# Performance work log

Hardware: AMD Instinct MI355X
Metric: run time of the kernel (lower is better)

The kernel has to match this reference:

```python
import jax, jax.numpy as jnp
import numpy as np

DIM = 768
NUM_HEADS = 1
AGENT_NUM = 4
HEAD_DIM = DIM // NUM_HEADS
SCALE = HEAD_DIM ** -0.5
B, N = 128, 196


def setup_inputs() -> dict:
    key = jax.random.key(0)
    ks = jax.random.split(key, 12)
    s = 0.02
    return {
        "x": jax.random.normal(ks[0], (B, N, DIM), jnp.float32),
        "attn_1": jax.random.normal(ks[1], (B, NUM_HEADS, AGENT_NUM, N), jnp.float32),
        "attn_2": jax.random.normal(ks[2], (B, NUM_HEADS, AGENT_NUM, N), jnp.float32),
        "agent_tk1": jax.random.normal(ks[3], (B, NUM_HEADS, AGENT_NUM, HEAD_DIM), jnp.float32),
        "agent_tk2": jax.random.normal(ks[4], (B, NUM_HEADS, AGENT_NUM, HEAD_DIM), jnp.float32),
        "W_qkv": jax.random.normal(ks[5], (DIM, 3 * DIM), jnp.float32) * s,
        "W_pool1": jax.random.normal(ks[6], (DIM, DIM // 2), jnp.float32) * s,
        "b_pool1": jnp.zeros((DIM // 2,), jnp.float32),
        "W_pool2": jax.random.normal(ks[7], (DIM // 2, NUM_HEADS * AGENT_NUM * DIM), jnp.float32) * s,
        "b_pool2": jnp.zeros((NUM_HEADS * AGENT_NUM * DIM,), jnp.float32),
        "W_proj": jax.random.normal(ks[8], (DIM, DIM), jnp.float32) * s,
        "b_proj": jnp.zeros((DIM,), jnp.float32),
    }


def reference(x, attn_1, attn_2, agent_tk1, agent_tk2,
              W_qkv, W_pool1, b_pool1, W_pool2, b_pool2, W_proj, b_proj):
    b, n, c = x.shape
    # qkv projection: (b, n, 3c) -> q, k, v each (b, n, c)
    qkv = x @ W_qkv
    q, k, v = jnp.split(qkv, 3, axis=-1)

    # agent tokens via pooling MLP on q (exact-erf GELU like torch nn.GELU)
    pooled = jax.nn.gelu(q @ W_pool1 + b_pool1, approximate=False) @ W_pool2 + b_pool2
    # mean over tokens -> (b, num_heads*agent_num*dim) == (b, agent_num*dim) since num_heads==1
    agent_tokens = pooled.mean(axis=1).reshape(b, AGENT_NUM, NUM_HEADS, HEAD_DIM)
    agent_tokens = agent_tokens.transpose(0, 2, 1, 3)  # (b, h, a, d)

    # split heads: (b, h, n, d)
    q = q.reshape(b, n, NUM_HEADS, HEAD_DIM).transpose(0, 2, 1, 3)
    k = k.reshape(b, n, NUM_HEADS, HEAD_DIM).transpose(0, 2, 1, 3)
    v = v.reshape(b, n, NUM_HEADS, HEAD_DIM).transpose(0, 2, 1, 3)

    # stage 1: agent attends to keys -> (b, h, a, n)
    agent_attn = jax.nn.softmax(jnp.einsum("bhad,bhnd->bhan", agent_tokens * SCALE, k), axis=-1)
    agent_rep = agent_attn

    # softmax blending with externally provided attn maps
    s = attn_1 + attn_2
    agent_attn = (agent_attn * jax.nn.softmax(s, axis=-1)
                  + agent_attn * jax.nn.softmax(s, axis=1)
                  + agent_attn) / 3.0

    agent_v = jnp.einsum("bhan,bhnd->bhad", agent_attn, v)  # (b, h, a, d)

    # blend agent tokens with external agent tokens
    t = agent_tk1 + agent_tk2
    agent_tokens = (agent_tokens * jax.nn.softmax(t, axis=-1)
                    + agent_tokens * jax.nn.softmax(t, axis=1)
                    + agent_tokens) / 3.0

    # stage 2: queries attend to agents -> (b, h, n, a)
    q_attn = jax.nn.softmax(jnp.einsum("bhnd,bhad->bhna", q * SCALE, agent_tokens), axis=-1)
    out = jnp.einsum("bhna,bhad->bhnd", q_attn, agent_v)  # (b, h, n, d)

    out = out.transpose(0, 2, 1, 3).reshape(b, n, c)
    out = out @ W_proj + b_proj
    return (out, agent_rep, agent_tokens)
```

## Files before the change

kernel.cpp:

```cpp
#include <hip/hip_runtime.h>
#include <hip/hip_bf16.h>
#include <math.h>

#define NB    128
#define NTOK  196
#define DIMC  768
#define AGN   4
#define SCALE_F 0.036084391824351614f

typedef __bf16  bf16x8  __attribute__((ext_vector_type(8)));
typedef float   f32x4   __attribute__((ext_vector_type(4)));
typedef unsigned short ushortx8 __attribute__((ext_vector_type(8)));
typedef unsigned short ushortx4 __attribute__((ext_vector_type(4)));

__device__ __forceinline__ unsigned short f2bf(float f) {
    union { float f; unsigned int u; } v; v.f = f;
    unsigned int r = v.u + 0x7fffu + ((v.u >> 16) & 1u);
    return (unsigned short)(r >> 16);
}
__device__ __forceinline__ float bf2f(unsigned short u) {
    union { unsigned int u; float f; } v; v.u = ((unsigned int)u) << 16;
    return v.f;
}
__device__ __forceinline__ void load_lds16(const void* g, void* l) {
    __builtin_amdgcn_global_load_lds(
        (const __attribute__((address_space(1))) unsigned int*)g,
        (__attribute__((address_space(3))) unsigned int*)l, 16, 0, 0);
}

template<int EPI>
__global__ __launch_bounds__(256) void gemm_bf16_k(
    const unsigned short* __restrict__ A, int lda,
    const unsigned short* __restrict__ Bt, int ldb,
    const float* __restrict__ bias,
    float* __restrict__ Cf, unsigned short* __restrict__ Cbf,
    int ldc, int K)
{
    __shared__ alignas(16) char lds[16384];

    const int tid  = threadIdx.x;
    const int lane = tid & 63;
    const int wv   = tid >> 6;
    const int wr   = wv >> 1, wc = wv & 1;
    const int row0 = blockIdx.y * 128;
    const int col0 = blockIdx.x * 128;

    const int c0 = wv * 2, c1 = wv * 2 + 1;
    const int srow = lane >> 2;
    const int skel = (lane & 3) << 3;
    const unsigned short* Ag0 = A  + (size_t)(row0 + c0*16 + srow) * lda + skel;
    const unsigned short* Ag1 = A  + (size_t)(row0 + c1*16 + srow) * lda + skel;
    const unsigned short* Bg0 = Bt + (size_t)(col0 + c0*16 + srow) * ldb + skel;
    const unsigned short* Bg1 = Bt + (size_t)(col0 + c1*16 + srow) * ldb + skel;
    char* lA0 = lds + c0 * 1024;
    char* lA1 = lds + c1 * 1024;
    char* lB0 = lds + 8192 + c0 * 1024;
    char* lB1 = lds + 8192 + c1 * 1024;

    f32x4 acc[4][4];
    #pragma unroll
    for (int m = 0; m < 4; m++)
        #pragma unroll
        for (int n = 0; n < 4; n++) acc[m][n] = (f32x4){0.f, 0.f, 0.f, 0.f};

    const int frow = lane & 15;
    const int kgrp = (lane >> 4) * 16;

    for (int bk = 0; bk < K; bk += 32) {
        __syncthreads();
        load_lds16(Ag0 + bk, lA0);
        load_lds16(Ag1 + bk, lA1);
        load_lds16(Bg0 + bk, lB0);
        load_lds16(Bg1 + bk, lB1);
        __syncthreads();

        bf16x8 af[4], bf[4];
        #pragma unroll
        for (int m = 0; m < 4; m++)
            af[m] = *(const bf16x8*)(lds + ((wr*64 + m*16 + frow) * 64 + kgrp));
        #pragma unroll
        for (int n = 0; n < 4; n++)
            bf[n] = *(const bf16x8*)(lds + 8192 + ((wc*64 + n*16 + frow) * 64 + kgrp));
        #pragma unroll
        for (int m = 0; m < 4; m++)
            #pragma unroll
            for (int n = 0; n < 4; n++)
                acc[m][n] = __builtin_amdgcn_mfma_f32_16x16x32_bf16(af[m], bf[n], acc[m][n], 0, 0, 0);
    }

    const int crow = (lane >> 4) << 2;
    #pragma unroll
    for (int n = 0; n < 4; n++) {
        const int col = col0 + wc*64 + n*16 + frow;
        const float bn = (EPI > 0) ? bias[col] : 0.f;
        #pragma unroll
        for (int m = 0; m < 4; m++) {
            #pragma unroll
            for (int r = 0; r < 4; r++) {
                const int row = row0 + wr*64 + m*16 + crow + r;
                float v = acc[m][n][r];
                if (EPI > 0) v += bn;
                if (EPI == 2) v = 0.5f * v * (1.f + erff(v * 0.7071067811865476f));
                if (EPI == 0) Cbf[(size_t)row * ldc + col] = f2bf(v);
                else          Cf [(size_t)row * ldc + col] = v;
            }
        }
    }
}

__global__ __launch_bounds__(256) void conv_k(const float* __restrict__ in,
                                              unsigned short* __restrict__ out)
{
    const size_t i = ((size_t)blockIdx.x * 256 + threadIdx.x) * 8;
    float4 v0 = *(const float4*)(in + i);
    float4 v1 = *(const float4*)(in + i + 4);
    ushortx8 o;
    o[0]=f2bf(v0.x); o[1]=f2bf(v0.y); o[2]=f2bf(v0.z); o[3]=f2bf(v0.w);
    o[4]=f2bf(v1.x); o[5]=f2bf(v1.y); o[6]=f2bf(v1.z); o[7]=f2bf(v1.w);
    *(ushortx8*)(out + i) = o;
}

__global__ __launch_bounds__(256) void tconv_k(const float* __restrict__ W,
                                               unsigned short* __restrict__ Wt,
                                               int K, int N)
{
    __shared__ float t[32][33];
    const int n0 = blockIdx.x * 32, k0 = blockIdx.y * 32;
    const int r = threadIdx.x >> 3;
    const int c = (threadIdx.x & 7) * 4;
    float4 v = *(const float4*)&W[(size_t)(k0 + r) * N + n0 + c];
    t[r][c] = v.x; t[r][c+1] = v.y; t[r][c+2] = v.z; t[r][c+3] = v.w;
    __syncthreads();
    ushortx4 o;
    o[0] = f2bf(t[c+0][r]); o[1] = f2bf(t[c+1][r]);
    o[2] = f2bf(t[c+2][r]); o[3] = f2bf(t[c+3][r]);
    *(ushortx4*)&Wt[(size_t)(n0 + r) * K + k0 + c] = o;
}

__global__ __launch_bounds__(384) void mean_k(const float* __restrict__ h1,
                                              float* __restrict__ mh)
{
    const int b = blockIdx.x, j = threadIdx.x;
    const float* p = h1 + (size_t)b * NTOK * 384 + j;
    float s = 0.f;
    for (int n = 0; n < NTOK; n++) s += p[(size_t)n * 384];
    mh[b * 384 + j] = s * (1.f / (float)NTOK);
}

__global__ __launch_bounds__(256) void pool2_k(const float* __restrict__ mh,
                                               const float* __restrict__ W2,
                                               const float* __restrict__ b2,
                                               float* __restrict__ ab)
{
    __shared__ float rows[8][384];
    const int tid = threadIdx.x;
    const int bb0 = blockIdx.y * 8;
    for (int i = tid; i < 8 * 384; i += 256)
        rows[i / 384][i % 384] = mh[(size_t)(bb0 + i / 384) * 384 + (i % 384)];
    __syncthreads();

    const int j = blockIdx.x * 256 + tid;
    const float bj = b2[j];
    float acc[8];
    #pragma unroll
    for (int r = 0; r < 8; r++) acc[r] = bj;
    for (int k = 0; k < 384; k++) {
        float w = W2[(size_t)k * 3072 + j];
        #pragma unroll
        for (int r = 0; r < 8; r++) acc[r] = fmaf(rows[r][k], w, acc[r]);
    }
    #pragma unroll
    for (int r = 0; r < 8; r++) ab[(size_t)(bb0 + r) * 3072 + j] = acc[r];
}

__device__ __forceinline__ float wred_max(float v) {
    #pragma unroll
    for (int o = 32; o; o >>= 1) v = fmaxf(v, __shfl_xor(v, o, 64));
    return v;
}
__device__ __forceinline__ float wred_sum(float v) {
    #pragma unroll
    for (int o = 32; o; o >>= 1) v += __shfl_xor(v, o, 64);
    return v;
}

__global__ __launch_bounds__(256) void stage1_k(
    const unsigned short* __restrict__ qkv, const float* __restrict__ agent_base,
    const float* __restrict__ attn1, const float* __restrict__ attn2,
    const float* __restrict__ tk1, const float* __restrict__ tk2,
    float* __restrict__ agent_v, float* __restrict__ at_blend,
    float* __restrict__ out_rep, float* __restrict__ out_at)
{
    __shared__ float at_s[AGN * DIMC];
    __shared__ float sc[AGN][NTOK];
    __shared__ float s2[AGN][NTOK];

    const int b = blockIdx.x, tid = threadIdx.x;
    for (int i = tid; i < AGN * DIMC; i += 256) at_s[i] = agent_base[(size_t)b * 3072 + i];
    __syncthreads();

    if (tid < NTOK) {
        const unsigned short* krow = qkv + (size_t)(b * NTOK + tid) * 2304 + 768;
        float s[AGN] = {0.f, 0.f, 0.f, 0.f};
        for (int d = 0; d < DIMC; d += 8) {
            ushortx8 kv = *(const ushortx8*)(krow + d);
            float kf[8];
            #pragma unroll
            for (int e = 0; e < 8; e++) kf[e] = bf2f(kv[e]);
            #pragma unroll
            for (int a = 0; a < AGN; a++) {
                const float* ap = at_s + a * DIMC + d;
                float t = 0.f;
                #pragma unroll
                for (int e = 0; e < 8; e++) t = fmaf(ap[e], kf[e], t);
                s[a] += t;
            }
        }
        #pragma unroll
        for (int a = 0; a < AGN; a++) {
            sc[a][tid] = s[a] * SCALE_F;
            s2[a][tid] = attn1[(size_t)(b*AGN + a)*NTOK + tid] + attn2[(size_t)(b*AGN + a)*NTOK + tid];
        }
    }
    __syncthreads();

    const int w = tid >> 6, l = tid & 63;
    {
        const int a = w;
        float m = -1e30f;
        for (int i = l; i < NTOK; i += 64) m = fmaxf(m, sc[a][i]);
        m = wred_max(m);
        float ss = 0.f;
        for (int i = l; i < NTOK; i += 64) { float e = expf(sc[a][i] - m); sc[a][i] = e; ss += e; }
        ss = wred_sum(ss);
        float inv = 1.f / ss;
        for (int i = l; i < NTOK; i += 64) {
            float p = sc[a][i] * inv;
            sc[a][i] = p;
            out_rep[(size_t)(b*AGN + a)*NTOK + i] = p;
        }
        float m2 = -1e30f;
        for (int i = l; i < NTOK; i += 64) m2 = fmaxf(m2, s2[a][i]);
        m2 = wred_max(m2);
        float ss2 = 0.f;
        for (int i = l; i < NTOK; i += 64) { float e = expf(s2[a][i] - m2); s2[a][i] = e; ss2 += e; }
        ss2 = wred_sum(ss2);
        float inv2 = 1.f / ss2;
        for (int i = l; i < NTOK; i += 64)
            s2[a][i] = sc[a][i] * (s2[a][i] * inv2 + 2.f) * (1.f / 3.f);
    }
    __syncthreads();

    for (int d = tid; d < DIMC; d += 256) {
        float av[AGN] = {0.f, 0.f, 0.f, 0.f};
        const unsigned short* vcol = qkv + (size_t)b * NTOK * 2304 + 1536 + d;
        for (int n = 0; n < NTOK; n++) {
            float vv = bf2f(vcol[(size_t)n * 2304]);
            #pragma unroll
            for (int a = 0; a < AGN; a++) av[a] = fmaf(s2[a][n], vv, av[a]);
        }
        #pragma unroll
        for (int a = 0; a < AGN; a++) agent_v[(size_t)(b*AGN + a)*DIMC + d] = av[a];
    }

    {
        const int a = w;
        float tv[12];
        float m = -1e30f;
        #pragma unroll
        for (int i = 0; i < 12; i++) {
            int d = l + i * 64;
            tv[i] = tk1[(size_t)(b*AGN + a)*DIMC + d] + tk2[(size_t)(b*AGN + a)*DIMC + d];
            m = fmaxf(m, tv[i]);
        }
        m = wred_max(m);
        float ss = 0.f;
        #pragma unroll
        for (int i = 0; i < 12; i++) { tv[i] = expf(tv[i] - m); ss += tv[i]; }
        ss = wred_sum(ss);
        float inv = 1.f / ss;
        #pragma unroll
        for (int i = 0; i < 12; i++) {
            int d = l + i * 64;
            float ab = at_s[a*DIMC + d] * (tv[i] * inv + 2.f) * (1.f / 3.f);
            at_blend[(size_t)(b*AGN + a)*DIMC + d] = ab;
            out_at[(size_t)(b*AGN + a)*DIMC + d] = ab;
        }
    }
}

__global__ __launch_bounds__(256) void stage2_k(
    const unsigned short* __restrict__ qkv, const float* __restrict__ at_blend,
    const float* __restrict__ agent_v, unsigned short* __restrict__ out_attn_bf)
{
    __shared__ float atb[AGN * DIMC];
    __shared__ float av[AGN * DIMC];
    __shared__ float qa[NTOK][AGN];

    const int b = blockIdx.x, tid = threadIdx.x;
    for (int i = tid; i < AGN * DIMC; i += 256) {
        atb[i] = at_blend[(size_t)b * 3072 + i];
        av[i]  = agent_v[(size_t)b * 3072 + i];
    }
    __syncthreads();

    if (tid < NTOK) {
        const unsigned short* qrow = qkv + (size_t)(b * NTOK + tid) * 2304;
        float s[AGN] = {0.f, 0.f, 0.f, 0.f};
        for (int d = 0; d < DIMC; d += 8) {
            ushortx8 qv = *(const ushortx8*)(qrow + d);
            float qf[8];
            #pragma unroll
            for (int e = 0; e < 8; e++) qf[e] = bf2f(qv[e]);
            #pragma unroll
            for (int a = 0; a < AGN; a++) {
                const float* ap = atb + a * DIMC + d;
                float t = 0.f;
                #pragma unroll
                for (int e = 0; e < 8; e++) t = fmaf(ap[e], qf[e], t);
                s[a] += t;
            }
        }
        #pragma unroll
        for (int a = 0; a < AGN; a++) s[a] *= SCALE_F;
        float m = fmaxf(fmaxf(s[0], s[1]), fmaxf(s[2], s[3]));
        float e[AGN]; float ss = 0.f;
        #pragma unroll
        for (int a = 0; a < AGN; a++) { e[a] = expf(s[a] - m); ss += e[a]; }
        float inv = 1.f / ss;
        #pragma unroll
        for (int a = 0; a < AGN; a++) qa[tid][a] = e[a] * inv;
    }
    __syncthreads();

    for (int n = 0; n < NTOK; n++) {
        const float p0 = qa[n][0], p1 = qa[n][1], p2 = qa[n][2], p3 = qa[n][3];
        for (int d = tid; d < DIMC; d += 256) {
            float o = p0*av[d] + p1*av[DIMC + d] + p2*av[2*DIMC + d] + p3*av[3*DIMC + d];
            out_attn_bf[(size_t)(b * NTOK + n) * DIMC + d] = f2bf(o);
        }
    }
}

extern "C" void kernel_launch(void* const* d_in, const int* in_sizes, int n_in,
                              void* d_out, int out_size, void* d_ws, size_t ws_size,
                              hipStream_t stream)
{
    const float* x     = (const float*)d_in[0];
    const float* attn1 = (const float*)d_in[1];
    const float* attn2 = (const float*)d_in[2];
    const float* tk1   = (const float*)d_in[3];
    const float* tk2   = (const float*)d_in[4];
    const float* Wqkv  = (const float*)d_in[5];
    const float* Wp1   = (const float*)d_in[6];
    const float* bp1   = (const float*)d_in[7];
    const float* Wp2   = (const float*)d_in[8];
    const float* bp2   = (const float*)d_in[9];
    const float* Wproj = (const float*)d_in[10];
    const float* bproj = (const float*)d_in[11];

    float* out     = (float*)d_out;
    float* out_rep = out + (size_t)NB * NTOK * DIMC;
    float* out_at  = out_rep + (size_t)NB * AGN * NTOK;

    char* ws = (char*)d_ws;
    unsigned short* qkvbf = (unsigned short*)ws;
    ws += (size_t)NB * NTOK * 2304 * 2;
    unsigned short* abuf = (unsigned short*)ws;
    ws += (size_t)NB * NTOK * DIMC * 2;
    float* h1 = (float*)ws;
    ws += (size_t)NB * NTOK * 384 * 4;
    unsigned short* Wqkvt = (unsigned short*)ws;  ws += (size_t)2304 * 768 * 2;
    unsigned short* Wp1t  = (unsigned short*)ws;  ws += (size_t)384 * 768 * 2;
    unsigned short* Wprojt= (unsigned short*)ws;  ws += (size_t)768 * 768 * 2;
    float* meanh1     = (float*)ws;  ws += (size_t)NB * 384 * 4;
    float* agent_base = (float*)ws;  ws += (size_t)NB * 3072 * 4;
    float* at_blend   = (float*)ws;  ws += (size_t)NB * 3072 * 4;
    float* agent_v    = (float*)ws;  ws += (size_t)NB * 3072 * 4;

    unsigned short* xbf = abuf;
    unsigned short* out_attn_bf = abuf;

    dim3 blk(256);

    conv_k<<<dim3(9408), blk, 0, stream>>>(x, xbf);
    tconv_k<<<dim3(2304/32, 768/32), blk, 0, stream>>>(Wqkv, Wqkvt, 768, 2304);
    tconv_k<<<dim3(384/32, 768/32), blk, 0, stream>>>(Wp1, Wp1t, 768, 384);
    tconv_k<<<dim3(768/32, 768/32), blk, 0, stream>>>(Wproj, Wprojt, 768, 768);

    gemm_bf16_k<0><<<dim3(18, 196), blk, 0, stream>>>(xbf, DIMC, Wqkvt, DIMC,
                                                      nullptr, nullptr, qkvbf, 2304, DIMC);
    gemm_bf16_k<2><<<dim3(3, 196), blk, 0, stream>>>(qkvbf, 2304, Wp1t, DIMC,
                                                     bp1, h1, nullptr, 384, DIMC);
    mean_k<<<dim3(NB), dim3(384), 0, stream>>>(h1, meanh1);
    pool2_k<<<dim3(12, 16), blk, 0, stream>>>(meanh1, Wp2, bp2, agent_base);
    stage1_k<<<dim3(NB), blk, 0, stream>>>(qkvbf, agent_base, attn1, attn2, tk1, tk2,
                                           agent_v, at_blend, out_rep, out_at);
    stage2_k<<<dim3(NB), blk, 0, stream>>>(qkvbf, at_blend, agent_v, out_attn_bf);
    gemm_bf16_k<1><<<dim3(6, 196), blk, 0, stream>>>(out_attn_bf, DIMC, Wprojt, DIMC,
                                                     bproj, out, nullptr, DIMC, DIMC);
}
```

Measured before the change: 576.0 us.

## Apply output projection to agent values before stage2, plus XCD remap and split reductions

Uses linearity to project the four agent value vectors per batch through W_proj (a tiny 512-row GEMM) instead of projecting all 25k token rows. Stage2 then writes final fp32 output directly as a softmax-weighted mix of projected agent values, split over four token chunks per batch. This removes the large final GEMM and the bf16 intermediate. Also adds XCD-aware workgroup remapping in the GEMM, splits the stage1/stage2 dot products across four lanes with shuffle reduction, and widens mean_k. The bias is folded in correctly since the softmax weights sum to one, and agent values are now rounded to bf16 before projection.

Measured after the change: 494.9 us. -14.1%, faster.

```diff
diff --git a/kernel.cpp b/kernel.cpp
--- a/kernel.cpp
+++ b/kernel.cpp
@@ -38,12 +38,19 @@
 {
     __shared__ alignas(16) char lds[16384];
 
+    const int nwg = gridDim.x * gridDim.y;
+    const int id  = blockIdx.y * gridDim.x + blockIdx.x;
+    const int q8  = nwg >> 3, r8 = nwg & 7;
+    const int xcd = id & 7, off = id >> 3;
+    const int nid = (xcd < r8 ? xcd * (q8 + 1) : r8 * (q8 + 1) + (xcd - r8) * q8) + off;
+    const int bx = nid % gridDim.x, by = nid / gridDim.x;
+
     const int tid  = threadIdx.x;
     const int lane = tid & 63;
     const int wv   = tid >> 6;
     const int wr   = wv >> 1, wc = wv & 1;
-    const int row0 = blockIdx.y * 128;
-    const int col0 = blockIdx.x * 128;
+    const int row0 = by * 128;
+    const int col0 = bx * 128;
 
     const int c0 = wv * 2, c1 = wv * 2 + 1;
     const int srow = lane >> 2;
@@ -137,14 +144,20 @@
     *(ushortx4*)&Wt[(size_t)(n0 + r) * K + k0 + c] = o;
 }
 
-__global__ __launch_bounds__(384) void mean_k(const float* __restrict__ h1,
+__global__ __launch_bounds__(128) void mean_k(const float* __restrict__ h1,
                                               float* __restrict__ mh)
 {
-    const int b = blockIdx.x, j = threadIdx.x;
+    const int b = blockIdx.x;
+    const int j = blockIdx.y * 128 + threadIdx.x;
     const float* p = h1 + (size_t)b * NTOK * 384 + j;
-    float s = 0.f;
-    for (int n = 0; n < NTOK; n++) s += p[(size_t)n * 384];
-    mh[b * 384 + j] = s * (1.f / (float)NTOK);
+    float s0 = 0.f, s1 = 0.f, s2 = 0.f, s3 = 0.f;
+    for (int n = 0; n < 196; n += 4) {
+        s0 += p[(size_t)(n+0) * 384];
+        s1 += p[(size_t)(n+1) * 384];
+        s2 += p[(size_t)(n+2) * 384];
+        s3 += p[(size_t)(n+3) * 384];
+    }
+    mh[b * 384 + j] = (s0 + s1 + s2 + s3) * (1.f / 196.f);
 }
 
 __global__ __launch_bounds__(256) void pool2_k(const float* __restrict__ mh,
@@ -164,6 +177,7 @@
     float acc[8];
     #pragma unroll
     for (int r = 0; r < 8; r++) acc[r] = bj;
+    #pragma unroll 4
     for (int k = 0; k < 384; k++) {
         float w = W2[(size_t)k * 3072 + j];
         #pragma unroll
@@ -188,7 +202,7 @@
     const unsigned short* __restrict__ qkv, const float* __restrict__ agent_base,
     const float* __restrict__ attn1, const float* __restrict__ attn2,
     const float* __restrict__ tk1, const float* __restrict__ tk2,
-    float* __restrict__ agent_v, float* __restrict__ at_blend,
+    unsigned short* __restrict__ agent_v_bf, float* __restrict__ at_blend,
     float* __restrict__ out_rep, float* __restrict__ out_at)
 {
     __shared__ float at_s[AGN * DIMC];
@@ -199,17 +213,18 @@
     for (int i = tid; i < AGN * DIMC; i += 256) at_s[i] = agent_base[(size_t)b * 3072 + i];
     __syncthreads();
 
-    if (tid < NTOK) {
-        const unsigned short* krow = qkv + (size_t)(b * NTOK + tid) * 2304 + 768;
-        float s[AGN] = {0.f, 0.f, 0.f, 0.f};
-        for (int d = 0; d < DIMC; d += 8) {
+    for (int tt = tid; tt < NTOK * 4; tt += 256) {
+        const int tok = tt >> 2, qo = tt & 3;
+        const unsigned short* krow = qkv + (size_t)(b * NTOK + tok) * 2304 + 768 + qo * 192;
+        float s[4] = {0.f, 0.f, 0.f, 0.f};
+        for (int d = 0; d < 192; d += 8) {
             ushortx8 kv = *(const ushortx8*)(krow + d);
             float kf[8];
             #pragma unroll
             for (int e = 0; e < 8; e++) kf[e] = bf2f(kv[e]);
             #pragma unroll
-            for (int a = 0; a < AGN; a++) {
-                const float* ap = at_s + a * DIMC + d;
+            for (int a = 0; a < 4; a++) {
+                const float* ap = at_s + a * DIMC + qo * 192 + d;
                 float t = 0.f;
                 #pragma unroll
                 for (int e = 0; e < 8; e++) t = fmaf(ap[e], kf[e], t);
@@ -217,10 +232,11 @@
             }
         }
         #pragma unroll
-        for (int a = 0; a < AGN; a++) {
-            sc[a][tid] = s[a] * SCALE_F;
-            s2[a][tid] = attn1[(size_t)(b*AGN + a)*NTOK + tid] + attn2[(size_t)(b*AGN + a)*NTOK + tid];
-        }
+        for (int o = 1; o <= 2; o <<= 1)
+            #pragma unroll
+            for (int a = 0; a < 4; a++) s[a] += __shfl_xor(s[a], o, 64);
+        sc[qo][tok] = s[qo] * SCALE_F;
+        s2[qo][tok] = attn1[(size_t)(b*AGN + qo)*NTOK + tok] + attn2[(size_t)(b*AGN + qo)*NTOK + tok];
     }
     __syncthreads();
 
@@ -260,7 +276,8 @@
             for (int a = 0; a < AGN; a++) av[a] = fmaf(s2[a][n], vv, av[a]);
         }
         #pragma unroll
-        for (int a = 0; a < AGN; a++) agent_v[(size_t)(b*AGN + a)*DIMC + d] = av[a];
+        for (int a = 0; a < AGN; a++)
+            agent_v_bf[(size_t)(b*AGN + a)*DIMC + d] = f2bf(av[a]);
     }
 
     {
@@ -291,30 +308,33 @@
 
 __global__ __launch_bounds__(256) void stage2_k(
     const unsigned short* __restrict__ qkv, const float* __restrict__ at_blend,
-    const float* __restrict__ agent_v, unsigned short* __restrict__ out_attn_bf)
+    const float* __restrict__ avw, float* __restrict__ out)
 {
     __shared__ float atb[AGN * DIMC];
-    __shared__ float av[AGN * DIMC];
-    __shared__ float qa[NTOK][AGN];
-
-    const int b = blockIdx.x, tid = threadIdx.x;
+    __shared__ float aw[AGN * DIMC];
+    __shared__ float qa[49][AGN];
+
+    const int b = blockIdx.y, chunk = blockIdx.x, tid = threadIdx.x;
     for (int i = tid; i < AGN * DIMC; i += 256) {
         atb[i] = at_blend[(size_t)b * 3072 + i];
-        av[i]  = agent_v[(size_t)b * 3072 + i];
-    }
-    __syncthreads();
-
-    if (tid < NTOK) {
-        const unsigned short* qrow = qkv + (size_t)(b * NTOK + tid) * 2304;
-        float s[AGN] = {0.f, 0.f, 0.f, 0.f};
-        for (int d = 0; d < DIMC; d += 8) {
+        aw[i]  = avw[(size_t)b * 3072 + i];
+    }
+    __syncthreads();
+
+    if (tid < 196) {
+        const int tl = tid >> 2;
+        const int qo = tid & 3;
+        const int tok = chunk * 49 + tl;
+        const unsigned short* qrow = qkv + (size_t)(b * NTOK + tok) * 2304 + qo * 192;
+        float s[4] = {0.f, 0.f, 0.f, 0.f};
+        for (int d = 0; d < 192; d += 8) {
             ushortx8 qv = *(const ushortx8*)(qrow + d);
             float qf[8];
             #pragma unroll
             for (int e = 0; e < 8; e++) qf[e] = bf2f(qv[e]);
             #pragma unroll
-            for (int a = 0; a < AGN; a++) {
-                const float* ap = atb + a * DIMC + d;
+            for (int a = 0; a < 4; a++) {
+                const float* ap = atb + a * DIMC + qo * 192 + d;
                 float t = 0.f;
                 #pragma unroll
                 for (int e = 0; e < 8; e++) t = fmaf(ap[e], qf[e], t);
@@ -322,22 +342,24 @@
             }
         }
         #pragma unroll
-        for (int a = 0; a < AGN; a++) s[a] *= SCALE_F;
+        for (int o = 1; o <= 2; o <<= 1)
+            #pragma unroll
+            for (int a = 0; a < 4; a++) s[a] += __shfl_xor(s[a], o, 64);
+        #pragma unroll
+        for (int a = 0; a < 4; a++) s[a] *= SCALE_F;
         float m = fmaxf(fmaxf(s[0], s[1]), fmaxf(s[2], s[3]));
         float e[AGN]; float ss = 0.f;
         #pragma unroll
-        for (int a = 0; a < AGN; a++) { e[a] = expf(s[a] - m); ss += e[a]; }
-        float inv = 1.f / ss;
-        #pragma unroll
-        for (int a = 0; a < AGN; a++) qa[tid][a] = e[a] * inv;
-    }
-    __syncthreads();
-
-    for (int n = 0; n < NTOK; n++) {
-        const float p0 = qa[n][0], p1 = qa[n][1], p2 = qa[n][2], p3 = qa[n][3];
+        for (int a = 0; a < 4; a++) { e[a] = expf(s[a] - m); ss += e[a]; }
+        qa[tl][qo] = e[qo] / ss;
+    }
+    __syncthreads();
+
+    for (int nn = 0; nn < 49; nn++) {
+        const float p0 = qa[nn][0], p1 = qa[nn][1], p2 = qa[nn][2], p3 = qa[nn][3];
+        const size_t rowo = (size_t)(b * NTOK + chunk * 49 + nn) * DIMC;
         for (int d = tid; d < DIMC; d += 256) {
-            float o = p0*av[d] + p1*av[DIMC + d] + p2*av[2*DIMC + d] + p3*av[3*DIMC + d];
-            out_attn_bf[(size_t)(b * NTOK + n) * DIMC + d] = f2bf(o);
+            out[rowo + d] = p0*aw[d] + p1*aw[DIMC + d] + p2*aw[2*DIMC + d] + p3*aw[3*DIMC + d];
         }
     }
 }
@@ -366,7 +388,7 @@
     char* ws = (char*)d_ws;
     unsigned short* qkvbf = (unsigned short*)ws;
     ws += (size_t)NB * NTOK * 2304 * 2;
-    unsigned short* abuf = (unsigned short*)ws;
+    unsigned short* xbf = (unsigned short*)ws;
     ws += (size_t)NB * NTOK * DIMC * 2;
     float* h1 = (float*)ws;
     ws += (size_t)NB * NTOK * 384 * 4;
@@ -376,10 +398,8 @@
     float* meanh1     = (float*)ws;  ws += (size_t)NB * 384 * 4;
     float* agent_base = (float*)ws;  ws += (size_t)NB * 3072 * 4;
     float* at_blend   = (float*)ws;  ws += (size_t)NB * 3072 * 4;
-    float* agent_v    = (float*)ws;  ws += (size_t)NB * 3072 * 4;
-
-    unsigned short* xbf = abuf;
-    unsigned short* out_attn_bf = abuf;
+    unsigned short* agent_v_bf = (unsigned short*)ws;  ws += (size_t)NB * AGN * DIMC * 2;
+    float* AVW        = (float*)ws;  ws += (size_t)NB * AGN * DIMC * 4;
 
     dim3 blk(256);
 
@@ -392,11 +412,11 @@
                                                       nullptr, nullptr, qkvbf, 2304, DIMC);
     gemm_bf16_k<2><<<dim3(3, 196), blk, 0, stream>>>(qkvbf, 2304, Wp1t, DIMC,
                                                      bp1, h1, nullptr, 384, DIMC);
-    mean_k<<<dim3(NB), dim3(384), 0, stream>>>(h1, meanh1);
+    mean_k<<<dim3(NB, 3), dim3(128), 0, stream>>>(h1, meanh1);
     pool2_k<<<dim3(12, 16), blk, 0, stream>>>(meanh1, Wp2, bp2, agent_base);
     stage1_k<<<dim3(NB), blk, 0, stream>>>(qkvbf, agent_base, attn1, attn2, tk1, tk2,
-                                           agent_v, at_blend, out_rep, out_at);
-    stage2_k<<<dim3(NB), blk, 0, stream>>>(qkvbf, at_blend, agent_v, out_attn_bf);
-    gemm_bf16_k<1><<<dim3(6, 196), blk, 0, stream>>>(out_attn_bf, DIMC, Wprojt, DIMC,
-                                                     bproj, out, nullptr, DIMC, DIMC);
-}
+                                           agent_v_bf, at_blend, out_rep, out_at);
+    gemm_bf16_k<1><<<dim3(6, 4), blk, 0, stream>>>(agent_v_bf, DIMC, Wprojt, DIMC,
+                                                   bproj, AVW, nullptr, DIMC, DIMC);
+    stage2_k<<<dim3(4, NB), blk, 0, stream>>>(qkvbf, at_blend, AVW, out);
+}
```
